# Kernel tuning notes

Measured on AMD Instinct MI355X. Metric: run time of the kernel, lower is better.

The kernel has to match this reference:

```python
import jax, jax.numpy as jnp
import numpy as np

G = 8
NEIGHBORS = 9
EPS = 1e-5


def grid_sample_bilinear_border(img, grid):
    # img: [B, C, H, W], grid: [B, Hg, Wg, 2] with (x, y) in [-1, 1]
    # matches torch.nn.functional.grid_sample(mode='bilinear', padding_mode='border', align_corners=False)
    B, C, H, W = img.shape
    gx, gy = grid[..., 0], grid[..., 1]
    ix = jnp.clip(((gx + 1.0) * W - 1.0) * 0.5, 0.0, W - 1.0)
    iy = jnp.clip(((gy + 1.0) * H - 1.0) * 0.5, 0.0, H - 1.0)
    x0 = jnp.floor(ix); y0 = jnp.floor(iy)
    x1 = x0 + 1.0;      y1 = y0 + 1.0
    w00 = (x1 - ix) * (y1 - iy)
    w01 = (ix - x0) * (y1 - iy)
    w10 = (x1 - ix) * (iy - y0)
    w11 = (ix - x0) * (iy - y0)
    x0i = jnp.clip(x0, 0, W - 1).astype(jnp.int32)
    x1i = jnp.clip(x1, 0, W - 1).astype(jnp.int32)
    y0i = jnp.clip(y0, 0, H - 1).astype(jnp.int32)
    y1i = jnp.clip(y1, 0, H - 1).astype(jnp.int32)

    def gather(im, yy, xx):  # im [C,H,W], yy/xx [Hg,Wg] -> [C,Hg,Wg]
        return im[:, yy, xx]

    g = jax.vmap(gather)
    out = (g(img, y0i, x0i) * w00[:, None]
         + g(img, y0i, x1i) * w01[:, None]
         + g(img, y1i, x0i) * w10[:, None]
         + g(img, y1i, x1i) * w11[:, None])
    return out  # [B, C, Hg, Wg]


def pconv(x, w):
    # 1x1x1 conv3d (no bias): x [B,Cin,D,H,W], w [Cout,Cin]
    return jnp.einsum('bcdhw,oc->bodhw', x, w)


def bn_relu(x, gamma, beta):
    # BatchNorm3d (training-mode batch stats, biased variance) + ReLU
    mean = jnp.mean(x, axis=(0, 2, 3, 4), keepdims=True)
    var = jnp.var(x, axis=(0, 2, 3, 4), keepdims=True)
    xn = (x - mean) * jax.lax.rsqrt(var + EPS)
    return jax.nn.relu(xn * gamma.reshape(1, -1, 1, 1, 1) + beta.reshape(1, -1, 1, 1, 1))


def setup_inputs() -> dict:
    key = jax.random.key(0)
    ks = jax.random.split(key, 8)
    B, C, H, W = 2, 64, 256, 320
    ref_feature = jax.random.normal(ks[0], (B, C, H, W), dtype=jnp.float32)
    grid = jax.random.uniform(ks[1], (B, NEIGHBORS * H, W, 2), dtype=jnp.float32,
                              minval=-1.0, maxval=1.0)
    s0 = 1.0 / np.sqrt(G)
    w0 = jax.random.uniform(ks[2], (16, G), jnp.float32, -s0, s0)
    g0 = jnp.ones((16,), jnp.float32); b0 = jnp.zeros((16,), jnp.float32)
    s1 = 1.0 / np.sqrt(16)
    w1 = jax.random.uniform(ks[3], (8, 16), jnp.float32, -s1, s1)
    g1 = jnp.ones((8,), jnp.float32); b1 = jnp.zeros((8,), jnp.float32)
    s2 = 1.0 / np.sqrt(8)
    ws = jax.random.uniform(ks[4], (1, 8), jnp.float32, -s2, s2)
    bs = jax.random.uniform(ks[5], (1,), jnp.float32, -s2, s2)
    return {"ref_feature": ref_feature, "grid": grid,
            "w0": w0, "g0": g0, "b0": b0,
            "w1": w1, "g1": g1, "b1": b1,
            "ws": ws, "bs": bs}


def reference(ref_feature, grid, w0, g0, b0, w1, g1, b1, ws, bs):
    B, C, H, W = ref_feature.shape
    x = grid_sample_bilinear_border(ref_feature, grid)          # [B, C, 9H, W]
    ref = ref_feature.reshape(B, G, C // G, H, W)               # [B, G, C/G, H, W]
    x = x.reshape(B, G, C // G, NEIGHBORS, H, W)
    x = jnp.mean(x * ref[:, :, :, None], axis=2)                # [B, G, 9, H, W]
    x = bn_relu(pconv(x, w0), g0, b0)                           # [B, 16, 9, H, W]
    x = bn_relu(pconv(x, w1), g1, b1)                           # [B, 8, 9, H, W]
    s = pconv(x, ws) + bs.reshape(1, -1, 1, 1, 1)               # [B, 1, 9, H, W]
    return jax.nn.sigmoid(jnp.squeeze(s, axis=1))               # [B, 9, H, W]
```

## Files before the change

### kernel.cpp

```cpp
#include <hip/hip_runtime.h>
#include <math.h>


constexpr int   Bc  = 2;
constexpr int   Cc  = 64;
constexpr int   Hc  = 256;
constexpr int   Wc  = 320;
constexpr int   NBc = 9;
constexpr int   HWc = Hc * Wc;
constexpr int   NPIX = Bc * HWc;
constexpr int   NPT  = Bc * NBc * HWc;
constexpr float EPSV = 1e-5f;

constexpr int NBLK_S = NPIX / 32;
constexpr int NBT4   = NPT / 1024;

constexpr size_t OFF_FEATB = 0;
constexpr size_t OFF_SB    = OFF_FEATB + (size_t)NPIX * 32;
constexpr size_t OFF_P2    = 0;
constexpr size_t OFF_PAR2  = OFF_P2 + (size_t)NBT4 * 16;
constexpr size_t OFF_TOT   = OFF_PAR2 + 64;

__device__ __forceinline__ unsigned short f2bf_rne(float v) {
  unsigned int u = __float_as_uint(v);
  unsigned int r = (u + 0x7fffu + ((u >> 16) & 1u)) >> 16;
  return (unsigned short)r;
}
__device__ __forceinline__ void unpack8(uint4 u, float f[8]) {
  f[0] = __uint_as_float(u.x << 16);
  f[1] = __uint_as_float(u.x & 0xffff0000u);
  f[2] = __uint_as_float(u.y << 16);
  f[3] = __uint_as_float(u.y & 0xffff0000u);
  f[4] = __uint_as_float(u.z << 16);
  f[5] = __uint_as_float(u.z & 0xffff0000u);
  f[6] = __uint_as_float(u.w << 16);
  f[7] = __uint_as_float(u.w & 0xffff0000u);
}
__device__ __forceinline__ float dot8(const float s[8], float4 wa, float4 wb) {
  return s[0] * wa.x + s[1] * wa.y + s[2] * wa.z + s[3] * wa.w +
         s[4] * wb.x + s[5] * wb.y + s[6] * wb.z + s[7] * wb.w;
}
__device__ __forceinline__ void addf4(float4& a, const float4 v) {
  a.x += v.x; a.y += v.y; a.z += v.z; a.w += v.w;
}

__global__ __launch_bounds__(256) void k_transpose(
    const float* __restrict__ feat, unsigned short* __restrict__ featB) {
  __shared__ float lds[64][65];
  const int tid  = threadIdx.x;
  const int b    = blockIdx.x / (HWc / 64);
  const int tile = blockIdx.x % (HWc / 64);
  const int hw0  = tile * 64;
  const int p    = tid & 63;
  const int ty   = tid >> 6;

  const float* src = feat + (size_t)b * Cc * HWc + hw0 + p;
#pragma unroll
  for (int c0 = 0; c0 < 64; c0 += 4) {
    lds[c0 + ty][p] = src[(size_t)(c0 + ty) * HWc];
  }
  __syncthreads();
  const int ch = tid & 63;
  unsigned short* dst = featB + ((size_t)b * HWc + hw0) * 64 + ch;
#pragma unroll
  for (int p0 = 0; p0 < 64; p0 += 4) {
    dst[(size_t)(p0 + ty) * 64] = f2bf_rne(lds[ch][p0 + ty]);
  }
}

__global__ __launch_bounds__(256) void k_sample(
    const float* __restrict__ grid, const unsigned short* __restrict__ featB,
    unsigned short* __restrict__ sOut, float* __restrict__ partM) {
  const int tid = threadIdx.x;
  const int cid = blockIdx.x * 32 + (tid >> 3);
  const int j   = tid & 7;
  const int b   = cid / HWc;
  const int hw  = cid - b * HWc;
  const int h   = hw / Wc;
  const int w   = hw - h * Wc;

  const uint4* fbAll = (const uint4*)featB;
  const uint4 ur = fbAll[(size_t)cid * 8 + j];
  float r[8];
  unpack8(ur, r);

  const uint4* fb = fbAll + (size_t)b * HWc * 8;

  float macc[8];
#pragma unroll
  for (int m = 0; m < 8; ++m) macc[m] = 0.f;
  float msum = 0.f;

#pragma unroll 3
  for (int n = 0; n < NBc; ++n) {
    const size_t gi = ((((size_t)b * NBc + n) * Hc + h) * Wc + w) * 2;
    const float2 g2 = *(const float2*)(grid + gi);
    float ix = ((g2.x + 1.f) * (float)Wc - 1.f) * 0.5f;
    float iy = ((g2.y + 1.f) * (float)Hc - 1.f) * 0.5f;
    ix = fminf(fmaxf(ix, 0.f), (float)(Wc - 1));
    iy = fminf(fmaxf(iy, 0.f), (float)(Hc - 1));
    const float x0f = floorf(ix), y0f = floorf(iy);
    const float fx = ix - x0f, fy = iy - y0f;
    const int x0 = (int)x0f, y0 = (int)y0f;
    const int x1 = min(x0 + 1, Wc - 1), y1 = min(y0 + 1, Hc - 1);
    const float w00 = (1.f - fx) * (1.f - fy);
    const float w01 = fx * (1.f - fy);
    const float w10 = (1.f - fx) * fy;
    const float w11 = fx * fy;

    const uint4 u00 = fb[(size_t)(y0 * Wc + x0) * 8 + j];
    const uint4 u01 = fb[(size_t)(y0 * Wc + x1) * 8 + j];
    const uint4 u10 = fb[(size_t)(y1 * Wc + x0) * 8 + j];
    const uint4 u11 = fb[(size_t)(y1 * Wc + x1) * 8 + j];
    float a[8], c[8], d[8], e[8];
    unpack8(u00, a);
    unpack8(u01, c);
    unpack8(u10, d);
    unpack8(u11, e);

    float s = 0.f;
#pragma unroll
    for (int k = 0; k < 8; ++k) {
      s += (w00 * a[k] + w01 * c[k] + w10 * d[k] + w11 * e[k]) * r[k];
    }
    s *= 0.125f;

    const size_t pt = ((size_t)b * NBc + n) * HWc + hw;
    sOut[pt * 8 + j] = f2bf_rne(s);

    macc[0] += s * s;
#pragma unroll
    for (int m = 1; m < 8; ++m) macc[m] += s * __shfl_xor(s, m);
    msum += s;
  }

#pragma unroll
  for (int m = 0; m < 8; ++m) {
    macc[m] += __shfl_xor(macc[m], 8);
    macc[m] += __shfl_xor(macc[m], 16);
    macc[m] += __shfl_xor(macc[m], 32);
  }
  msum += __shfl_xor(msum, 8);
  msum += __shfl_xor(msum, 16);
  msum += __shfl_xor(msum, 32);

  __shared__ float mred[4][72];
  const int lane = tid & 63, wid = tid >> 6;
  if (lane < 8) {
#pragma unroll
    for (int m = 0; m < 8; ++m) mred[wid][lane * 9 + m] = macc[m];
    mred[wid][lane * 9 + 8] = msum;
  }
  __syncthreads();
  if (tid < 72) {
    partM[(size_t)tid * NBLK_S + blockIdx.x] =
        mred[0][tid] + mred[1][tid] + mred[2][tid] + mred[3][tid];
  }
}

__global__ __launch_bounds__(256) void k_reduce1a(
    const float* __restrict__ partM, float* __restrict__ tot) {
  const int tid = threadIdx.x;
  const float4* base = (const float4*)(partM + (size_t)blockIdx.x * NBLK_S);
  float4 a0 = base[tid];
  float4 a1 = base[tid + 256];
  float4 a2 = base[tid + 512];
  float4 a3 = base[tid + 768];
  float4 a4 = base[tid + 1024];
  addf4(a0, a1); addf4(a2, a3); addf4(a0, a2); addf4(a0, a4);
  float v = (a0.x + a0.y) + (a0.z + a0.w);
#pragma unroll
  for (int off = 32; off; off >>= 1) v += __shfl_xor(v, off);
  __shared__ float red[4];
  if ((tid & 63) == 0) red[tid >> 6] = v;
  __syncthreads();
  if (tid == 0) tot[blockIdx.x] = (red[0] + red[1]) + (red[2] + red[3]);
}

__device__ __forceinline__ void bn1_prologue(
    const float* __restrict__ tot, const float* __restrict__ w0,
    const float* __restrict__ w1, const float* __restrict__ g0,
    const float* __restrict__ b0, float* tots, float* a1sS, float* w0ps,
    float* c1vs, float* w1ts) {
  const int tid = threadIdx.x;
  if (tid < 72) tots[tid] = tot[tid];
  __syncthreads();
  if (tid < 16) {
    float wr[8];
    float mean = 0.f, ey2 = 0.f;
#pragma unroll
    for (int jj = 0; jj < 8; ++jj) {
      wr[jj] = w0[tid * 8 + jj];
      mean += wr[jj] * tots[jj * 9 + 8];
    }
#pragma unroll
    for (int jj = 0; jj < 8; ++jj) {
#pragma unroll
      for (int kk = 0; kk < 8; ++kk) {
        ey2 += wr[jj] * wr[kk] * tots[jj * 9 + (jj ^ kk)];
      }
    }
    const float invN = 1.f / (float)NPT;
    mean *= invN;
    ey2 *= invN;
    const float var = ey2 - mean * mean;
    const float a = g0[tid] * rsqrtf(var + EPSV);
    a1sS[tid] = a;
    c1vs[tid] = b0[tid] - mean * a;
  }
  __syncthreads();
  if (tid < 128) {
    w0ps[tid] = a1sS[tid >> 3] * w0[tid];
    w1ts[(tid & 15) * 8 + (tid >> 4)] = w1[tid];
  }
  __syncthreads();
}

__global__ __launch_bounds__(256) void k_stats2(
    const unsigned short* __restrict__ sB, const float* __restrict__ tot,
    const float* __restrict__ w0, const float* __restrict__ w1,
    const float* __restrict__ g0, const float* __restrict__ b0,
    float* __restrict__ part2) {
  __shared__ float tots[72], a1sS[16], w0ps[128], c1vs[16], w1ts[128];
  __shared__ float red[64];
  const int tid = threadIdx.x;
  bn1_prologue(tot, w0, w1, g0, b0, tots, a1sS, w0ps, c1vs, w1ts);

  const uint4* src = (const uint4*)sB + (size_t)blockIdx.x * 1024 + tid;
  float s0[8], s1[8], s2[8], s3[8];
  unpack8(src[0], s0);
  unpack8(src[256], s1);
  unpack8(src[512], s2);
  unpack8(src[768], s3);

  float z0[8], z1[8], z2[8], z3[8];
#pragma unroll
  for (int o = 0; o < 8; ++o) { z0[o] = 0.f; z1[o] = 0.f; z2[o] = 0.f; z3[o] = 0.f; }
#pragma unroll
  for (int c = 0; c < 16; ++c) {
    const float4 wa = *(const float4*)(w0ps + c * 8);
    const float4 wb = *(const float4*)(w0ps + c * 8 + 4);
    const float cc = c1vs[c];
    const float4 ta = *(const float4*)(w1ts + c * 8);
    const float4 tb = *(const float4*)(w1ts + c * 8 + 4);
    const float xa = fmaxf(dot8(s0, wa, wb) + cc, 0.f);
    const float xb = fmaxf(dot8(s1, wa, wb) + cc, 0.f);
    const float xc = fmaxf(dot8(s2, wa, wb) + cc, 0.f);
    const float xd = fmaxf(dot8(s3, wa, wb) + cc, 0.f);
    z0[0] += ta.x * xa; z0[1] += ta.y * xa; z0[2] += ta.z * xa; z0[3] += ta.w * xa;
    z0[4] += tb.x * xa; z0[5] += tb.y * xa; z0[6] += tb.z * xa; z0[7] += tb.w * xa;
    z1[0] += ta.x * xb; z1[1] += ta.y * xb; z1[2] += ta.z * xb; z1[3] += ta.w * xb;
    z1[4] += tb.x * xb; z1[5] += tb.y * xb; z1[6] += tb.z * xb; z1[7] += tb.w * xb;
    z2[0] += ta.x * xc; z2[1] += ta.y * xc; z2[2] += ta.z * xc; z2[3] += ta.w * xc;
    z2[4] += tb.x * xc; z2[5] += tb.y * xc; z2[6] += tb.z * xc; z2[7] += tb.w * xc;
    z3[0] += ta.x * xd; z3[1] += ta.y * xd; z3[2] += ta.z * xd; z3[3] += ta.w * xd;
    z3[4] += tb.x * xd; z3[5] += tb.y * xd; z3[6] += tb.z * xd; z3[7] += tb.w * xd;
  }

  const int wid = tid >> 6;
#pragma unroll
  for (int o = 0; o < 8; ++o) {
    float v = (z0[o] + z1[o]) + (z2[o] + z3[o]);
    float v2 = (z0[o] * z0[o] + z1[o] * z1[o]) + (z2[o] * z2[o] + z3[o] * z3[o]);
#pragma unroll
    for (int off = 32; off; off >>= 1) {
      v += __shfl_xor(v, off);
      v2 += __shfl_xor(v2, off);
    }
    if ((tid & 63) == 0) {
      red[wid * 16 + o] = v;
      red[wid * 16 + 8 + o] = v2;
    }
  }
  __syncthreads();
  if (tid < 16) {
    part2[blockIdx.x * 16 + tid] =
        red[tid] + red[16 + tid] + red[32 + tid] + red[48 + tid];
  }
}

__global__ __launch_bounds__(256) void k_reduce2(
    const float* __restrict__ part2, const float* __restrict__ g1,
    const float* __restrict__ b1, const float* __restrict__ wsW,
    const float* __restrict__ bs, float* __restrict__ par2) {
  __shared__ float red[1024], totz[16];
  const int tid = threadIdx.x;
  {
    const int cq = tid & 3, chk = tid >> 2;
    const float4* base = (const float4*)part2;
    float4 a0 = make_float4(0.f, 0.f, 0.f, 0.f), a1 = a0, a2 = a0, a3 = a0;
    int r = chk;
    while (r + 192 < NBT4) {
      addf4(a0, base[(size_t)(r)*4 + cq]);
      addf4(a1, base[(size_t)(r + 64) * 4 + cq]);
      addf4(a2, base[(size_t)(r + 128) * 4 + cq]);
      addf4(a3, base[(size_t)(r + 192) * 4 + cq]);
      r += 256;
    }
    for (; r < NBT4; r += 64) addf4(a0, base[(size_t)r * 4 + cq]);
    addf4(a0, a1); addf4(a2, a3); addf4(a0, a2);
    red[chk * 16 + cq * 4 + 0] = a0.x;
    red[chk * 16 + cq * 4 + 1] = a0.y;
    red[chk * 16 + cq * 4 + 2] = a0.z;
    red[chk * 16 + cq * 4 + 3] = a0.w;
  }
  __syncthreads();
  if (tid < 16) {
    float v = 0.f;
#pragma unroll
    for (int k = 0; k < 64; ++k) v += red[k * 16 + tid];
    totz[tid] = v;
  }
  __syncthreads();
  if (tid < 8) {
    const float invN = 1.f / (float)NPT;
    const float mean = totz[tid] * invN;
    const float var = totz[8 + tid] * invN - mean * mean;
    const float a = g1[tid] * rsqrtf(var + EPSV);
    par2[tid * 4 + 0] = a;
    par2[tid * 4 + 1] = b1[tid] - mean * a;
    par2[tid * 4 + 2] = wsW[tid];
    par2[tid * 4 + 3] = 0.f;
  }
  if (tid == 8) par2[32] = bs[0];
}

__global__ __launch_bounds__(256) void k_final(
    const unsigned short* __restrict__ sB, const float* __restrict__ tot,
    const float* __restrict__ w0, const float* __restrict__ w1,
    const float* __restrict__ g0, const float* __restrict__ b0,
    const float* __restrict__ par2, float* __restrict__ out) {
  __shared__ float tots[72], a1sS[16], w0ps[128], c1vs[16], w1ts[128];
  __shared__ float w2s[33];
  const int tid = threadIdx.x;
  if (tid >= 160 && tid < 193) w2s[tid - 160] = par2[tid - 160];
  bn1_prologue(tot, w0, w1, g0, b0, tots, a1sS, w0ps, c1vs, w1ts);

  const uint4* src = (const uint4*)sB + (size_t)blockIdx.x * 1024 + tid;
  float s0[8], s1[8], s2[8], s3[8];
  unpack8(src[0], s0);
  unpack8(src[256], s1);
  unpack8(src[512], s2);
  unpack8(src[768], s3);

  float z0[8], z1[8], z2[8], z3[8];
#pragma unroll
  for (int o = 0; o < 8; ++o) { z0[o] = 0.f; z1[o] = 0.f; z2[o] = 0.f; z3[o] = 0.f; }
#pragma unroll
  for (int c = 0; c < 16; ++c) {
    const float4 wa = *(const float4*)(w0ps + c * 8);
    const float4 wb = *(const float4*)(w0ps + c * 8 + 4);
    const float cc = c1vs[c];
    const float4 ta = *(const float4*)(w1ts + c * 8);
    const float4 tb = *(const float4*)(w1ts + c * 8 + 4);
    const float xa = fmaxf(dot8(s0, wa, wb) + cc, 0.f);
    const float xb = fmaxf(dot8(s1, wa, wb) + cc, 0.f);
    const float xc = fmaxf(dot8(s2, wa, wb) + cc, 0.f);
    const float xd = fmaxf(dot8(s3, wa, wb) + cc, 0.f);
    z0[0] += ta.x * xa; z0[1] += ta.y * xa; z0[2] += ta.z * xa; z0[3] += ta.w * xa;
    z0[4] += tb.x * xa; z0[5] += tb.y * xa; z0[6] += tb.z * xa; z0[7] += tb.w * xa;
    z1[0] += ta.x * xb; z1[1] += ta.y * xb; z1[2] += ta.z * xb; z1[3] += ta.w * xb;
    z1[4] += tb.x * xb; z1[5] += tb.y * xb; z1[6] += tb.z * xb; z1[7] += tb.w * xb;
    z2[0] += ta.x * xc; z2[1] += ta.y * xc; z2[2] += ta.z * xc; z2[3] += ta.w * xc;
    z2[4] += tb.x * xc; z2[5] += tb.y * xc; z2[6] += tb.z * xc; z2[7] += tb.w * xc;
    z3[0] += ta.x * xd; z3[1] += ta.y * xd; z3[2] += ta.z * xd; z3[3] += ta.w * xd;
    z3[4] += tb.x * xd; z3[5] += tb.y * xd; z3[6] += tb.z * xd; z3[7] += tb.w * xd;
  }

  const float bsr = w2s[32];
  float r0 = bsr, r1 = bsr, r2 = bsr, r3 = bsr;
#pragma unroll
  for (int o = 0; o < 8; ++o) {
    const float4 pr = *(const float4*)(w2s + o * 4);
    r0 += pr.z * fmaxf(fmaf(pr.x, z0[o], pr.y), 0.f);
    r1 += pr.z * fmaxf(fmaf(pr.x, z1[o], pr.y), 0.f);
    r2 += pr.z * fmaxf(fmaf(pr.x, z2[o], pr.y), 0.f);
    r3 += pr.z * fmaxf(fmaf(pr.x, z3[o], pr.y), 0.f);
  }
  float* op = out + (size_t)blockIdx.x * 1024 + tid;
  op[0]   = 1.f / (1.f + __expf(-r0));
  op[256] = 1.f / (1.f + __expf(-r1));
  op[512] = 1.f / (1.f + __expf(-r2));
  op[768] = 1.f / (1.f + __expf(-r3));
}

extern "C" void kernel_launch(void* const* d_in, const int* in_sizes, int n_in,
                              void* d_out, int out_size, void* d_ws,
                              size_t ws_size, hipStream_t stream) {
  const float* feat = (const float*)d_in[0];
  const float* grid = (const float*)d_in[1];
  const float* w0 = (const float*)d_in[2];
  const float* g0 = (const float*)d_in[3];
  const float* b0 = (const float*)d_in[4];
  const float* w1 = (const float*)d_in[5];
  const float* g1 = (const float*)d_in[6];
  const float* b1 = (const float*)d_in[7];
  const float* wsW = (const float*)d_in[8];
  const float* bs = (const float*)d_in[9];
  float* out = (float*)d_out;

  float* wsf = (float*)d_ws;
  unsigned short* featB = (unsigned short*)(wsf + OFF_FEATB);
  unsigned short* sB    = (unsigned short*)(wsf + OFF_SB);
  float* part2 = wsf + OFF_P2;
  float* par2  = wsf + OFF_PAR2;
  float* tot   = wsf + OFF_TOT;
  float* partM = out;

  k_transpose<<<Bc * (HWc / 64), 256, 0, stream>>>(feat, featB);
  k_sample<<<NBLK_S, 256, 0, stream>>>(grid, featB, sB, partM);
  k_reduce1a<<<72, 256, 0, stream>>>(partM, tot);
  k_stats2<<<NBT4, 256, 0, stream>>>(sB, tot, w0, w1, g0, b0, part2);
  k_reduce2<<<1, 256, 0, stream>>>(part2, g1, b1, wsW, bs, par2);
  k_final<<<NBT4, 256, 0, stream>>>(sB, tot, w0, w1, g0, b0, par2, out);
}
```

Before: 226.7 us.

## Fold BN2 stat reduction into final kernel, pack transpose stores, relayout partials

Removes the single-block k_reduce2 launch: every k_final block now reduces the part2 partials itself and builds the BN2 parameters in shared memory. The transpose kernel writes two bf16 channels per 32-bit store instead of 16-bit stores. The sample kernel's per-block partial sums move to a block-major layout so each block's write is contiguous. The cost is redundant reduction work and extra part2 reads in every final block, plus strided reads in reduce1a.

```diff
diff --git a/kernel.cpp b/kernel.cpp
--- a/kernel.cpp
+++ b/kernel.cpp
@@ -18,8 +18,7 @@
 constexpr size_t OFF_FEATB = 0;
 constexpr size_t OFF_SB    = OFF_FEATB + (size_t)NPIX * 32;
 constexpr size_t OFF_P2    = 0;
-constexpr size_t OFF_PAR2  = OFF_P2 + (size_t)NBT4 * 16;
-constexpr size_t OFF_TOT   = OFF_PAR2 + 64;
+constexpr size_t OFF_TOT   = OFF_P2 + (size_t)NBT4 * 16;
 
 __device__ __forceinline__ unsigned short f2bf_rne(float v) {
   unsigned int u = __float_as_uint(v);
@@ -60,11 +59,16 @@
     lds[c0 + ty][p] = src[(size_t)(c0 + ty) * HWc];
   }
   __syncthreads();
-  const int ch = tid & 63;
-  unsigned short* dst = featB + ((size_t)b * HWc + hw0) * 64 + ch;
-#pragma unroll
-  for (int p0 = 0; p0 < 64; p0 += 4) {
-    dst[(size_t)(p0 + ty) * 64] = f2bf_rne(lds[ch][p0 + ty]);
+  const int ch2 = tid & 31;
+  const int py0 = tid >> 5;
+  unsigned int* dstu =
+      (unsigned int*)(featB + ((size_t)b * HWc + hw0) * 64);
+#pragma unroll
+  for (int q = 0; q < 8; ++q) {
+    const int p1 = q * 8 + py0;
+    const unsigned int lo = f2bf_rne(lds[ch2 * 2][p1]);
+    const unsigned int hi = f2bf_rne(lds[ch2 * 2 + 1][p1]);
+    dstu[(size_t)p1 * 32 + ch2] = lo | (hi << 16);
   }
 }
 
@@ -153,7 +157,7 @@
   }
   __syncthreads();
   if (tid < 72) {
-    partM[(size_t)tid * NBLK_S + blockIdx.x] =
+    partM[(size_t)blockIdx.x * 72 + tid] =
         mred[0][tid] + mred[1][tid] + mred[2][tid] + mred[3][tid];
   }
 }
@@ -161,20 +165,19 @@
 __global__ __launch_bounds__(256) void k_reduce1a(
     const float* __restrict__ partM, float* __restrict__ tot) {
   const int tid = threadIdx.x;
-  const float4* base = (const float4*)(partM + (size_t)blockIdx.x * NBLK_S);
-  float4 a0 = base[tid];
-  float4 a1 = base[tid + 256];
-  float4 a2 = base[tid + 512];
-  float4 a3 = base[tid + 768];
-  float4 a4 = base[tid + 1024];
-  addf4(a0, a1); addf4(a2, a3); addf4(a0, a2); addf4(a0, a4);
-  float v = (a0.x + a0.y) + (a0.z + a0.w);
+  const int c = blockIdx.x;
+  float acc[5] = {0.f, 0.f, 0.f, 0.f, 0.f};
+#pragma unroll
+  for (int k = 0; k < 20; ++k) {
+    acc[k % 5] += partM[(size_t)(tid + 256 * k) * 72 + c];
+  }
+  float v = ((acc[0] + acc[1]) + (acc[2] + acc[3])) + acc[4];
 #pragma unroll
   for (int off = 32; off; off >>= 1) v += __shfl_xor(v, off);
   __shared__ float red[4];
   if ((tid & 63) == 0) red[tid >> 6] = v;
   __syncthreads();
-  if (tid == 0) tot[blockIdx.x] = (red[0] + red[1]) + (red[2] + red[3]);
+  if (tid == 0) tot[c] = (red[0] + red[1]) + (red[2] + red[3]);
 }
 
 __device__ __forceinline__ void bn1_prologue(
@@ -279,11 +282,15 @@
   }
 }
 
-__global__ __launch_bounds__(256) void k_reduce2(
-    const float* __restrict__ part2, const float* __restrict__ g1,
+__global__ __launch_bounds__(256) void k_final(
+    const unsigned short* __restrict__ sB, const float* __restrict__ tot,
+    const float* __restrict__ part2, const float* __restrict__ w0,
+    const float* __restrict__ w1, const float* __restrict__ g0,
+    const float* __restrict__ b0, const float* __restrict__ g1,
     const float* __restrict__ b1, const float* __restrict__ wsW,
-    const float* __restrict__ bs, float* __restrict__ par2) {
-  __shared__ float red[1024], totz[16];
+    const float* __restrict__ bs, float* __restrict__ out) {
+  __shared__ float tots[72], a1sS[16], w0ps[128], c1vs[16], w1ts[128];
+  __shared__ float red2[1024], totz[16], w2s[33];
   const int tid = threadIdx.x;
   {
     const int cq = tid & 3, chk = tid >> 2;
@@ -299,16 +306,16 @@
     }
     for (; r < NBT4; r += 64) addf4(a0, base[(size_t)r * 4 + cq]);
     addf4(a0, a1); addf4(a2, a3); addf4(a0, a2);
-    red[chk * 16 + cq * 4 + 0] = a0.x;
-    red[chk * 16 + cq * 4 + 1] = a0.y;
-    red[chk * 16 + cq * 4 + 2] = a0.z;
-    red[chk * 16 + cq * 4 + 3] = a0.w;
+    red2[chk * 16 + cq * 4 + 0] = a0.x;
+    red2[chk * 16 + cq * 4 + 1] = a0.y;
+    red2[chk * 16 + cq * 4 + 2] = a0.z;
+    red2[chk * 16 + cq * 4 + 3] = a0.w;
   }
   __syncthreads();
   if (tid < 16) {
     float v = 0.f;
 #pragma unroll
-    for (int k = 0; k < 64; ++k) v += red[k * 16 + tid];
+    for (int k = 0; k < 64; ++k) v += red2[k * 16 + tid];
     totz[tid] = v;
   }
   __syncthreads();
@@ -317,23 +324,12 @@
     const float mean = totz[tid] * invN;
     const float var = totz[8 + tid] * invN - mean * mean;
     const float a = g1[tid] * rsqrtf(var + EPSV);
-    par2[tid * 4 + 0] = a;
-    par2[tid * 4 + 1] = b1[tid] - mean * a;
-    par2[tid * 4 + 2] = wsW[tid];
-    par2[tid * 4 + 3] = 0.f;
-  }
-  if (tid == 8) par2[32] = bs[0];
-}
-
-__global__ __launch_bounds__(256) void k_final(
-    const unsigned short* __restrict__ sB, const float* __restrict__ tot,
-    const float* __restrict__ w0, const float* __restrict__ w1,
-    const float* __restrict__ g0, const float* __restrict__ b0,
-    const float* __restrict__ par2, float* __restrict__ out) {
-  __shared__ float tots[72], a1sS[16], w0ps[128], c1vs[16], w1ts[128];
-  __shared__ float w2s[33];
-  const int tid = threadIdx.x;
-  if (tid >= 160 && tid < 193) w2s[tid - 160] = par2[tid - 160];
+    w2s[tid * 4 + 0] = a;
+    w2s[tid * 4 + 1] = b1[tid] - mean * a;
+    w2s[tid * 4 + 2] = wsW[tid];
+    w2s[tid * 4 + 3] = 0.f;
+  }
+  if (tid == 8) w2s[32] = bs[0];
   bn1_prologue(tot, w0, w1, g0, b0, tots, a1sS, w0ps, c1vs, w1ts);
 
   const uint4* src = (const uint4*)sB + (size_t)blockIdx.x * 1024 + tid;
@@ -403,7 +399,6 @@
   unsigned short* featB = (unsigned short*)(wsf + OFF_FEATB);
   unsigned short* sB    = (unsigned short*)(wsf + OFF_SB);
   float* part2 = wsf + OFF_P2;
-  float* par2  = wsf + OFF_PAR2;
   float* tot   = wsf + OFF_TOT;
   float* partM = out;
 
@@ -411,6 +406,6 @@
   k_sample<<<NBLK_S, 256, 0, stream>>>(grid, featB, sB, partM);
   k_reduce1a<<<72, 256, 0, stream>>>(partM, tot);
   k_stats2<<<NBT4, 256, 0, stream>>>(sB, tot, w0, w1, g0, b0, part2);
-  k_reduce2<<<1, 256, 0, stream>>>(part2, g1, b1, wsW, bs, par2);
-  k_final<<<NBT4, 256, 0, stream>>>(sB, tot, w0, w1, g0, b0, par2, out);
-}
+  k_final<<<NBT4, 256, 0, stream>>>(sB, tot, part2, w0, w1, g0, b0, g1, b1,
+                                    wsW, bs, out);
+}
```

Result: no change. 231.1 us (+2.0%).
